# Kernel optimization log

Measured on AMD Instinct MI355X. Metric: run time of the kernel, lower is better.

## Reference

```python
import jax, jax.numpy as jnp
import numpy as np

TEMPERATURE = 0.5
BATCH = 2048  # N = batch_size * world_size (world_size = 1)
FEAT = 128
EPS = 1e-8  # torch CosineSimilarity default eps


def _build_mask_indices(N):
    """Replicates mask_correlated_samples + the row-major boolean gather
    sim[mask].reshape(2N, -1). Returns static flat indices [2N, 2N-1]."""
    sub = np.ones((2 * N, 2 * N), dtype=bool)
    np.fill_diagonal(sub, False)
    idx = np.arange(N)
    sub[idx, N + idx] = False
    sub[N + idx, idx] = False
    mask = np.zeros((3 * N, 3 * N), dtype=bool)
    mask[:2 * N, :2 * N] = sub
    mask[idx, 2 * N + idx] = True
    mask[2 * N + idx, idx] = True
    flat = np.nonzero(mask.ravel())[0]  # row-major order, 2N*(2N-1) entries
    return flat.reshape(2 * N, 2 * N - 1)


_NEG_IDX = jnp.asarray(_build_mask_indices(BATCH), dtype=jnp.int32)


def setup_inputs() -> dict:
    key = jax.random.key(0)
    ka, kp, kn = jax.random.split(key, 3)
    return {
        "anchor": jax.random.normal(ka, (BATCH, FEAT), dtype=jnp.float32),
        "pos": jax.random.normal(kp, (BATCH, FEAT), dtype=jnp.float32),
        "neg": jax.random.normal(kn, (BATCH, FEAT), dtype=jnp.float32),
    }


def reference(anchor, pos, neg):
    N = anchor.shape[0]
    z = jnp.concatenate([anchor, pos, neg], axis=0)  # [3N, d]
    zn = z / jnp.maximum(jnp.linalg.norm(z, axis=1, keepdims=True), EPS)
    sim = (zn @ zn.T) / TEMPERATURE  # [3N, 3N]
    # positive pairs: diagonals at offset +/-2N (anchor<->neg pairs)
    sim_i_j = jnp.diagonal(sim, offset=2 * N)[:N]
    sim_j_i = jnp.diagonal(sim, offset=-2 * N)[:N]
    positive = jnp.concatenate([sim_i_j, sim_j_i]).reshape(2 * N, 1)
    # masked gather of negatives (static index table, row-major order)
    negative = jnp.take(sim.ravel(), _NEG_IDX)  # [2N, 2N-1]
    logits = jnp.concatenate([positive, negative], axis=1)  # [2N, 2N]
    # cross-entropy with label 0, reduction='sum', then / (2N)
    loss = jnp.sum(jax.nn.logsumexp(logits, axis=1) - logits[:, 0]) / (2 * N)
    return loss
```

## Files before the change

### kernel.cpp

```cpp
#include <hip/hip_runtime.h>
#include <hip/hip_bf16.h>

#define N_      2048
#define TWO_N   4096
#define DFEAT   128
#define SCALE   2.0f
#define BROWS   128
#define BCOLS   128
#define NT      (BCOLS / 16)
#define LDSTR   132
#define SC_L2E  2.8853900817779268f

typedef __attribute__((ext_vector_type(8))) short bf16x8;
typedef __attribute__((ext_vector_type(4))) float f32x4;

__global__ __launch_bounds__(256) void k_prep(const float* __restrict__ a,
                                              const float* __restrict__ p,
                                              const float* __restrict__ ng,
                                              __hip_bfloat16* __restrict__ zn16,
                                              float* __restrict__ dvec,
                                              float* __restrict__ accS,
                                              float* __restrict__ accP,
                                              float* __restrict__ out) {
  const int wave = threadIdx.x >> 6;
  const int lane = threadIdx.x & 63;
  const int row  = blockIdx.x * 4 + wave;

  if (threadIdx.x < 4)        accS[blockIdx.x * 4 + threadIdx.x] = 0.0f;
  else if (threadIdx.x < 6)   accP[blockIdx.x * 2 + threadIdx.x - 4] = 0.0f;
  if (blockIdx.x == 0 && threadIdx.x == 6) out[0] = 0.0f;

  if (row < N_) {
    float2 u = ((const float2*)(a  + (size_t)row * DFEAT))[lane];
    float2 w = ((const float2*)(ng + (size_t)row * DFEAT))[lane];
    float saa = u.x * u.x + u.y * u.y;
    float snn = w.x * w.x + w.y * w.y;
    float san = u.x * w.x + u.y * w.y;
#pragma unroll
    for (int m = 1; m < 64; m <<= 1) {
      saa += __shfl_xor(saa, m);
      snn += __shfl_xor(snn, m);
      san += __shfl_xor(san, m);
    }
    float na = fmaxf(sqrtf(saa), 1e-8f);
    float rn = 1.0f / na;
    __hip_bfloat162 h;
    h.x = __float2bfloat16(u.x * rn);
    h.y = __float2bfloat16(u.y * rn);
    ((__hip_bfloat162*)zn16)[row * (DFEAT / 2) + lane] = h;
    if (lane == 0)
      dvec[row] = SCALE * san / (na * fmaxf(sqrtf(snn), 1e-8f));
  } else {
    float2 v = ((const float2*)(p + (size_t)(row - N_) * DFEAT))[lane];
    float ss = v.x * v.x + v.y * v.y;
#pragma unroll
    for (int m = 1; m < 64; m <<= 1) ss += __shfl_xor(ss, m);
    float rn = 1.0f / fmaxf(sqrtf(ss), 1e-8f);
    __hip_bfloat162 h;
    h.x = __float2bfloat16(v.x * rn);
    h.y = __float2bfloat16(v.y * rn);
    ((__hip_bfloat162*)zn16)[row * (DFEAT / 2) + lane] = h;
  }
}

__global__ __launch_bounds__(256) void k_simsum(const __hip_bfloat16* __restrict__ zn16,
                                                float* __restrict__ accS,
                                                float* __restrict__ accP) {
  __shared__ __align__(16) short Bp[BCOLS * LDSTR];

  const int bx = blockIdx.x, by = blockIdx.y;
  const int wave = threadIdx.x >> 6;
  const int lane = threadIdx.x & 63;
  const int lr   = lane & 15;
  const int kg   = lane >> 4;
  const int rows_base = bx * BROWS + wave * 32;
  const int cb0 = by * BCOLS;
  const short* zs = (const short*)zn16;

  const bool hi = (bx >= 16);
  const int cls = (by == bx) ? 0
                : (!hi && by == bx + 16) ? 1
                : (hi && by == bx - 16) ? 2
                : (hi && by < bx - 16) ? 3
                : 4;

  bf16x8 a0[4], a1[4];
#pragma unroll
  for (int kk = 0; kk < 4; ++kk) {
    a0[kk] = *(const bf16x8*)(zs + (size_t)(rows_base + lr) * DFEAT + kk * 32 + kg * 8);
    a1[kk] = *(const bf16x8*)(zs + (size_t)(rows_base + 16 + lr) * DFEAT + kk * 32 + kg * 8);
  }

#pragma unroll
  for (int it = 0; it < 8; ++it) {
    const int g   = it * 256 + threadIdx.x;
    const int col = g >> 4;
    const int q   = g & 15;
    bf16x8 v = *(const bf16x8*)(zs + (size_t)(cb0 + col) * DFEAT + q * 8);
    *(bf16x8*)(&Bp[col * LDSTR + q * 8]) = v;
  }
  __syncthreads();

  int rrow[2][4], excl[2][4];
#pragma unroll
  for (int t = 0; t < 2; ++t)
#pragma unroll
    for (int j = 0; j < 4; ++j) {
      rrow[t][j] = rows_base + t * 16 + kg * 4 + j;
      excl[t][j] = (cls == 0) ? rrow[t][j]
                 : (cls == 1) ? rrow[t][j] + N_
                 : (cls == 2) ? rrow[t][j] - N_ : -1;
    }

  float acc1v[2][4] = {{0.f,0.f,0.f,0.f},{0.f,0.f,0.f,0.f}};
  float acc2v[2][4] = {{0.f,0.f,0.f,0.f},{0.f,0.f,0.f,0.f}};

  bf16x8 bcur[4], bnxt[4];
#pragma unroll
  for (int kk = 0; kk < 4; ++kk)
    bcur[kk] = *(const bf16x8*)(&Bp[lr * LDSTR + kk * 32 + kg * 8]);

#pragma unroll 2
  for (int ct = 0; ct < NT; ++ct) {
    const int ctn = (ct + 1 < NT) ? (ct + 1) : ct;
#pragma unroll
    for (int kk = 0; kk < 4; ++kk)
      bnxt[kk] = *(const bf16x8*)(&Bp[(ctn * 16 + lr) * LDSTR + kk * 32 + kg * 8]);

    f32x4 acc0 = {0.f, 0.f, 0.f, 0.f};
    f32x4 acc1 = {0.f, 0.f, 0.f, 0.f};
#pragma unroll
    for (int kk = 0; kk < 4; ++kk) {
      acc0 = __builtin_amdgcn_mfma_f32_16x16x32_bf16(a0[kk], bcur[kk], acc0, 0, 0, 0);
      acc1 = __builtin_amdgcn_mfma_f32_16x16x32_bf16(a1[kk], bcur[kk], acc1, 0, 0, 0);
    }

    const int c = cb0 + ct * 16 + lr;
    if (cls >= 3) {
#pragma unroll
      for (int j = 0; j < 4; ++j) {
        acc1v[0][j] += __builtin_amdgcn_exp2f(acc0[j] * SC_L2E);
        acc1v[1][j] += __builtin_amdgcn_exp2f(acc1[j] * SC_L2E);
      }
    } else if (cls == 2) {
#pragma unroll
      for (int j = 0; j < 4; ++j) {
        float e0 = __builtin_amdgcn_exp2f(acc0[j] * SC_L2E);
        e0 = (c == excl[0][j]) ? 0.0f : e0;
        if (c < excl[0][j]) acc2v[0][j] += e0; else acc1v[0][j] += e0;
        float e1 = __builtin_amdgcn_exp2f(acc1[j] * SC_L2E);
        e1 = (c == excl[1][j]) ? 0.0f : e1;
        if (c < excl[1][j]) acc2v[1][j] += e1; else acc1v[1][j] += e1;
      }
    } else {
#pragma unroll
      for (int j = 0; j < 4; ++j) {
        float e0 = __builtin_amdgcn_exp2f(acc0[j] * SC_L2E);
        acc1v[0][j] += (c == excl[0][j]) ? 0.0f : e0;
        float e1 = __builtin_amdgcn_exp2f(acc1[j] * SC_L2E);
        acc1v[1][j] += (c == excl[1][j]) ? 0.0f : e1;
      }
    }

#pragma unroll
    for (int kk = 0; kk < 4; ++kk) bcur[kk] = bnxt[kk];
  }

#pragma unroll
  for (int t = 0; t < 2; ++t)
#pragma unroll
    for (int j = 0; j < 4; ++j) {
      float v1 = acc1v[t][j], v2 = acc2v[t][j];
#pragma unroll
      for (int m = 1; m < 16; m <<= 1) {
        v1 += __shfl_xor(v1, m);
        if (cls == 2) v2 += __shfl_xor(v2, m);
      }
      if (lr == 0) {
        const int r = rrow[t][j];
        if (cls == 3)      atomicAdd(&accP[r - N_], v1);
        else               atomicAdd(&accS[r], v1);
        if (cls == 2)      atomicAdd(&accP[r - N_], v2);
      }
    }
}

__global__ __launch_bounds__(256) void k_final(const float* __restrict__ dvec,
                                               const float* __restrict__ accS,
                                               const float* __restrict__ accP,
                                               float* __restrict__ out) {
  __shared__ float red[4];
  __shared__ float DsumSh;
  const int tid  = threadIdx.x;
  const int wave = tid >> 6, lane = tid & 63;
  const int r    = blockIdx.x * 256 + tid;

  if (blockIdx.x == 15) {
    float s = 0.f;
#pragma unroll
    for (int k = 0; k < 8; ++k) s += __expf(dvec[tid + k * 256]);
#pragma unroll
    for (int m = 1; m < 64; m <<= 1) s += __shfl_xor(s, m);
    if (lane == 0) red[wave] = s;
    __syncthreads();
    if (tid == 0) DsumSh = red[0] + red[1] + red[2] + red[3];
    __syncthreads();
  }

  const float S = accS[r];
  float term;
  if (r < N_) {
    const float dv = dvec[r];
    term = __logf(2.0f * __expf(dv) + S) - dv;
  } else {
    const int i = r - N_;
    const float extra = (i < N_ - 1) ? accP[i + 1] : DsumSh;
    const float dv = dvec[i];
    term = __logf(__expf(dv) + S + extra) - dv;
  }

#pragma unroll
  for (int m = 1; m < 64; m <<= 1) term += __shfl_xor(term, m);
  if (lane == 0) red[wave] = term;
  __syncthreads();
  if (tid == 0)
    atomicAdd(out, (red[0] + red[1] + red[2] + red[3]) * (1.0f / (float)TWO_N));
}

extern "C" void kernel_launch(void* const* d_in, const int* in_sizes, int n_in,
                              void* d_out, int out_size, void* d_ws, size_t ws_size,
                              hipStream_t stream) {
  const float* a  = (const float*)d_in[0];
  const float* p  = (const float*)d_in[1];
  const float* ng = (const float*)d_in[2];

  char* ws = (char*)d_ws;
  __hip_bfloat16* zn16 = (__hip_bfloat16*)ws;
  float* dvec = (float*)(ws + (size_t)TWO_N * DFEAT * 2);
  float* accS = dvec + TWO_N;
  float* accP = accS + TWO_N;

  k_prep<<<TWO_N / 4, 256, 0, stream>>>(a, p, ng, zn16, dvec, accS, accP,
                                        (float*)d_out);
  k_simsum<<<dim3(TWO_N / BROWS, TWO_N / BCOLS), 256, 0, stream>>>(zn16, accS, accP);
  k_final<<<16, 256, 0, stream>>>(dvec, accS, accP, (float*)d_out);
}
```

Before: 23.15 us.

## Double per-wave row tile to 64 rows, reusing each B fragment across four MFMAs

Each block now covers 256 rows, so each wave handles 64 rows (four 16-row MFMA tiles) instead of 32, and each LDS B fragment feeds four MFMAs instead of two. The block-class logic is remapped so one row block spans two column blocks. The explicit register double-buffering of B fragments is dropped in favor of plain per-iteration loads. This cuts LDS and global B traffic per FLOP and halves the grid to 512 blocks, at the cost of more registers per thread and less latency hiding from prefetch.

```diff
diff --git a/kernel.cpp b/kernel.cpp
--- a/kernel.cpp
+++ b/kernel.cpp
@@ -5,7 +5,7 @@
 #define TWO_N   4096
 #define DFEAT   128
 #define SCALE   2.0f
-#define BROWS   128
+#define BROWS   256
 #define BCOLS   128
 #define NT      (BCOLS / 16)
 #define LDSTR   132
@@ -73,23 +73,24 @@
   const int lane = threadIdx.x & 63;
   const int lr   = lane & 15;
   const int kg   = lane >> 4;
-  const int rows_base = bx * BROWS + wave * 32;
+  const int rows_base = bx * BROWS + wave * 64;
   const int cb0 = by * BCOLS;
   const short* zs = (const short*)zn16;
 
-  const bool hi = (bx >= 16);
-  const int cls = (by == bx) ? 0
-                : (!hi && by == bx + 16) ? 1
-                : (hi && by == bx - 16) ? 2
-                : (hi && by < bx - 16) ? 3
+  const bool hi = (bx >= 8);
+  const int cls = (by == 2*bx || by == 2*bx + 1) ? 0
+                : (!hi && (by == 2*bx + 16 || by == 2*bx + 17)) ? 1
+                : (hi && (by == 2*bx - 16 || by == 2*bx - 15)) ? 2
+                : (hi && by < 2*bx - 16) ? 3
                 : 4;
 
-  bf16x8 a0[4], a1[4];
-#pragma unroll
-  for (int kk = 0; kk < 4; ++kk) {
-    a0[kk] = *(const bf16x8*)(zs + (size_t)(rows_base + lr) * DFEAT + kk * 32 + kg * 8);
-    a1[kk] = *(const bf16x8*)(zs + (size_t)(rows_base + 16 + lr) * DFEAT + kk * 32 + kg * 8);
-  }
+  bf16x8 a[4][4];
+#pragma unroll
+  for (int t = 0; t < 4; ++t)
+#pragma unroll
+    for (int kk = 0; kk < 4; ++kk)
+      a[t][kk] = *(const bf16x8*)(zs + (size_t)(rows_base + t * 16 + lr) * DFEAT
+                                  + kk * 32 + kg * 8);
 
 #pragma unroll
   for (int it = 0; it < 8; ++it) {
@@ -101,9 +102,9 @@
   }
   __syncthreads();
 
-  int rrow[2][4], excl[2][4];
-#pragma unroll
-  for (int t = 0; t < 2; ++t)
+  int rrow[4][4], excl[4][4];
+#pragma unroll
+  for (int t = 0; t < 4; ++t)
 #pragma unroll
     for (int j = 0; j < 4; ++j) {
       rrow[t][j] = rows_base + t * 16 + kg * 4 + j;
@@ -112,62 +113,53 @@
                  : (cls == 2) ? rrow[t][j] - N_ : -1;
     }
 
-  float acc1v[2][4] = {{0.f,0.f,0.f,0.f},{0.f,0.f,0.f,0.f}};
-  float acc2v[2][4] = {{0.f,0.f,0.f,0.f},{0.f,0.f,0.f,0.f}};
-
-  bf16x8 bcur[4], bnxt[4];
-#pragma unroll
-  for (int kk = 0; kk < 4; ++kk)
-    bcur[kk] = *(const bf16x8*)(&Bp[lr * LDSTR + kk * 32 + kg * 8]);
+  float acc1v[4][4] = {};
+  float acc2v[4][4] = {};
 
 #pragma unroll 2
   for (int ct = 0; ct < NT; ++ct) {
-    const int ctn = (ct + 1 < NT) ? (ct + 1) : ct;
+    bf16x8 b[4];
 #pragma unroll
     for (int kk = 0; kk < 4; ++kk)
-      bnxt[kk] = *(const bf16x8*)(&Bp[(ctn * 16 + lr) * LDSTR + kk * 32 + kg * 8]);
-
-    f32x4 acc0 = {0.f, 0.f, 0.f, 0.f};
-    f32x4 acc1 = {0.f, 0.f, 0.f, 0.f};
-#pragma unroll
-    for (int kk = 0; kk < 4; ++kk) {
-      acc0 = __builtin_amdgcn_mfma_f32_16x16x32_bf16(a0[kk], bcur[kk], acc0, 0, 0, 0);
-      acc1 = __builtin_amdgcn_mfma_f32_16x16x32_bf16(a1[kk], bcur[kk], acc1, 0, 0, 0);
-    }
+      b[kk] = *(const bf16x8*)(&Bp[(ct * 16 + lr) * LDSTR + kk * 32 + kg * 8]);
+
+    f32x4 acc[4] = {{0.f,0.f,0.f,0.f},{0.f,0.f,0.f,0.f},
+                    {0.f,0.f,0.f,0.f},{0.f,0.f,0.f,0.f}};
+#pragma unroll
+    for (int kk = 0; kk < 4; ++kk)
+#pragma unroll
+      for (int t = 0; t < 4; ++t)
+        acc[t] = __builtin_amdgcn_mfma_f32_16x16x32_bf16(a[t][kk], b[kk], acc[t], 0, 0, 0);
 
     const int c = cb0 + ct * 16 + lr;
     if (cls >= 3) {
 #pragma unroll
-      for (int j = 0; j < 4; ++j) {
-        acc1v[0][j] += __builtin_amdgcn_exp2f(acc0[j] * SC_L2E);
-        acc1v[1][j] += __builtin_amdgcn_exp2f(acc1[j] * SC_L2E);
-      }
+      for (int t = 0; t < 4; ++t)
+#pragma unroll
+        for (int j = 0; j < 4; ++j)
+          acc1v[t][j] += __builtin_amdgcn_exp2f(acc[t][j] * SC_L2E);
     } else if (cls == 2) {
 #pragma unroll
-      for (int j = 0; j < 4; ++j) {
-        float e0 = __builtin_amdgcn_exp2f(acc0[j] * SC_L2E);
-        e0 = (c == excl[0][j]) ? 0.0f : e0;
-        if (c < excl[0][j]) acc2v[0][j] += e0; else acc1v[0][j] += e0;
-        float e1 = __builtin_amdgcn_exp2f(acc1[j] * SC_L2E);
-        e1 = (c == excl[1][j]) ? 0.0f : e1;
-        if (c < excl[1][j]) acc2v[1][j] += e1; else acc1v[1][j] += e1;
-      }
+      for (int t = 0; t < 4; ++t)
+#pragma unroll
+        for (int j = 0; j < 4; ++j) {
+          float e = __builtin_amdgcn_exp2f(acc[t][j] * SC_L2E);
+          e = (c == excl[t][j]) ? 0.0f : e;
+          if (c < excl[t][j]) acc2v[t][j] += e; else acc1v[t][j] += e;
+        }
     } else {
 #pragma unroll
-      for (int j = 0; j < 4; ++j) {
-        float e0 = __builtin_amdgcn_exp2f(acc0[j] * SC_L2E);
-        acc1v[0][j] += (c == excl[0][j]) ? 0.0f : e0;
-        float e1 = __builtin_amdgcn_exp2f(acc1[j] * SC_L2E);
-        acc1v[1][j] += (c == excl[1][j]) ? 0.0f : e1;
-      }
-    }
-
-#pragma unroll
-    for (int kk = 0; kk < 4; ++kk) bcur[kk] = bnxt[kk];
-  }
-
-#pragma unroll
-  for (int t = 0; t < 2; ++t)
+      for (int t = 0; t < 4; ++t)
+#pragma unroll
+        for (int j = 0; j < 4; ++j) {
+          float e = __builtin_amdgcn_exp2f(acc[t][j] * SC_L2E);
+          acc1v[t][j] += (c == excl[t][j]) ? 0.0f : e;
+        }
+    }
+  }
+
+#pragma unroll
+  for (int t = 0; t < 4; ++t)
 #pragma unroll
     for (int j = 0; j < 4; ++j) {
       float v1 = acc1v[t][j], v2 = acc2v[t][j];
```

After: 26.27 us. 1.13x slower.
